# Performance work log

Hardware: AMD Instinct MI355X
Metric: run time of the kernel (lower is better)

## Reference

```python
import jax, jax.numpy as jnp
import numpy as np


def setup_inputs() -> dict:
    key = jax.random.key(0)
    kx, kA, kB, kC, kd = jax.random.split(key, 5)
    d_model, d_state = 2048, 16
    batch, seq_len = 2, 4096
    x = jax.random.normal(kx, (batch, seq_len, d_model), dtype=jnp.float32)
    # HiPPO-style init would be log(arange(1..N)); random positive works for the same math
    A_log = jax.random.uniform(kA, (d_model, d_state), dtype=jnp.float32)
    B = jax.random.normal(kB, (d_model, d_state), dtype=jnp.float32) * 0.02
    C = jax.random.normal(kC, (d_model, d_state), dtype=jnp.float32) * 0.02
    D = jnp.ones((d_model,), dtype=jnp.float32)
    delta = jax.random.uniform(kd, (d_model,), dtype=jnp.float32) * 0.01 + 0.005
    return {"x": x, "A_log": A_log, "B": B, "C": C, "D": D, "delta": delta}


def reference(x, A_log, B, C, D, delta):
    # x: (batch, seq_len, d_model); params per-channel diagonal SSM
    A = -jnp.exp(A_log)                      # (d_model, d_state)
    # zero-order-hold discretization
    A_bar = jnp.exp(delta[:, None] * A)      # (d_model, d_state)
    B_bar = delta[:, None] * B               # (d_model, d_state)

    batch, seq_len, d_model = x.shape
    d_state = A_bar.shape[-1]
    xT = jnp.swapaxes(x, 0, 1)               # (seq_len, batch, d_model)

    def step(h, x_t):
        # h: (batch, d_model, d_state); x_t: (batch, d_model)
        h = A_bar * h + B_bar * x_t[..., None]
        y_t = jnp.einsum('dn,bdn->bd', C, h)
        return h, y_t

    h0 = jnp.zeros((batch, d_model, d_state), dtype=x.dtype)
    _, ys = jax.lax.scan(step, h0, xT)       # ys: (seq_len, batch, d_model)
    y = jnp.swapaxes(ys, 0, 1)
    return y + D * x
```

## Files before the change

### kernel.cpp

```cpp
#include <hip/hip_runtime.h>

#define DM 2048
#define DS 16
#define BATCH 2
#define SEQ 4096
#define P (BATCH * DM)
#define UNR 8


__global__ __launch_bounds__(256) void k_params(const float* __restrict__ A_log,
                                                const float* __restrict__ B,
                                                const float* __restrict__ C,
                                                const float* __restrict__ delta,
                                                float* __restrict__ ws, int Lsteps) {
  int j = blockIdx.x * 256 + threadIdx.x;
  if (j >= DM * DS) return;
  int n = j / DM, d = j - n * DM;
  float dl = delta[d];
  float a = -expf(A_log[d * DS + n]);
  ws[j] = expf(dl * a);
  ws[DS * DM + j] = C[d * DS + n] * dl * B[d * DS + n];
  ws[2 * DS * DM + j] = expf(dl * a * (float)Lsteps);
}

__global__ __launch_bounds__(256) void k_local(const float* __restrict__ x,
                                               const float* __restrict__ ws,
                                               float* __restrict__ Hloc, int Lsteps) {
  int tid = blockIdx.x * 256 + threadIdx.x;
  int p = tid & (P - 1);
  int k = tid >> 12;
  int b = p >> 11;
  int d = p & (DM - 1);
  const float* Abar = ws;
  float ab[DS], g[DS];
#pragma unroll
  for (int n = 0; n < DS; n++) {
    ab[n] = Abar[n * DM + d];
    g[n] = 0.f;
  }
  const float* xp = x + ((size_t)b * SEQ + (size_t)k * Lsteps) * DM + d;
  for (int t = 0; t < Lsteps; t += UNR) {
    float xv[UNR];
#pragma unroll
    for (int j = 0; j < UNR; j++) xv[j] = xp[(size_t)j * DM];
#pragma unroll
    for (int j = 0; j < UNR; j++) {
#pragma unroll
      for (int n = 0; n < DS; n++) g[n] = fmaf(ab[n], g[n], xv[j]);
    }
    xp += (size_t)UNR * DM;
  }
  float* Hp = Hloc + (size_t)(k * DS) * P + p;
#pragma unroll
  for (int n = 0; n < DS; n++) Hp[n * P] = g[n];
}

__global__ __launch_bounds__(256) void k_scan(float* __restrict__ Hloc,
                                              const float* __restrict__ ws, int nc) {
  int tid = blockIdx.x * 256 + threadIdx.x;
  int p = tid & (P - 1);
  int n = tid >> 12;
  int d = p & (DM - 1);
  const float* PowL = ws + 2 * DS * DM;
  float pw = PowL[n * DM + d];
  float carry = 0.f;
  float* Hp = Hloc + (size_t)n * P + p;
  const size_t stride = (size_t)DS * P;
  for (int k0 = 0; k0 < nc; k0 += 16) {
    float v[16];
#pragma unroll
    for (int j = 0; j < 16; j++) v[j] = Hp[(size_t)(k0 + j) * stride];
#pragma unroll
    for (int j = 0; j < 16; j++) {
      Hp[(size_t)(k0 + j) * stride] = carry;
      carry = fmaf(pw, carry, v[j]);
    }
  }
}

__global__ __launch_bounds__(256) void k_final(const float* __restrict__ x,
                                               const float* __restrict__ ws,
                                               const float* __restrict__ Hloc,
                                               const float* __restrict__ Dp,
                                               float* __restrict__ out, int Lsteps) {
  int tid = blockIdx.x * 256 + threadIdx.x;
  int p = tid & (P - 1);
  int k = tid >> 12;
  int b = p >> 11;
  int d = p & (DM - 1);
  const float* Abar = ws;
  const float* CB = ws + DS * DM;
  float ab[DS], cb[DS], g[DS];
#pragma unroll
  for (int n = 0; n < DS; n++) {
    ab[n] = Abar[n * DM + d];
    cb[n] = CB[n * DM + d];
  }
  const float* Hp = Hloc + (size_t)(k * DS) * P + p;
#pragma unroll
  for (int n = 0; n < DS; n++) g[n] = Hp[n * P];
  float Dd = Dp[d];
  size_t off = ((size_t)b * SEQ + (size_t)k * Lsteps) * DM + d;
  const float* xp = x + off;
  float* yp = out + off;
  for (int t = 0; t < Lsteps; t += UNR) {
    float xv[UNR];
#pragma unroll
    for (int j = 0; j < UNR; j++) xv[j] = xp[(size_t)j * DM];
#pragma unroll
    for (int j = 0; j < UNR; j++) {
#pragma unroll
      for (int n = 0; n < DS; n++) g[n] = fmaf(ab[n], g[n], xv[j]);
      float acc = Dd * xv[j];
#pragma unroll
      for (int n = 0; n < DS; n++) acc = fmaf(cb[n], g[n], acc);
      yp[(size_t)j * DM] = acc;
    }
    xp += (size_t)UNR * DM;
    yp += (size_t)UNR * DM;
  }
}

extern "C" void kernel_launch(void* const* d_in, const int* in_sizes, int n_in,
                              void* d_out, int out_size, void* d_ws, size_t ws_size,
                              hipStream_t stream) {
  const float* x = (const float*)d_in[0];
  const float* A_log = (const float*)d_in[1];
  const float* B = (const float*)d_in[2];
  const float* C = (const float*)d_in[3];
  const float* Dp = (const float*)d_in[4];
  const float* delta = (const float*)d_in[5];
  float* out = (float*)d_out;
  float* ws = (float*)d_ws;

  size_t base = 3 * (size_t)DS * DM;
  int nc = 32;
  while (nc > 16 && (base + (size_t)nc * DS * P) * 4 > ws_size) nc >>= 1;
  int Lsteps = SEQ / nc;
  float* Hloc = ws + base;

  k_params<<<(DM * DS + 255) / 256, 256, 0, stream>>>(A_log, B, C, delta, ws, Lsteps);
  k_local<<<(nc * P) / 256, 256, 0, stream>>>(x, ws, Hloc, Lsteps);
  k_scan<<<(DS * P) / 256, 256, 0, stream>>>(Hloc, ws, nc);
  k_final<<<(nc * P) / 256, 256, 0, stream>>>(x, ws, Hloc, Dp, out, Lsteps);
}
```

Baseline: 53.25 us.

## Fuse local, scan and final phases into one cooperative kernel with register-cached x

Merges the three chunked-scan kernels into one cooperative kernel separated by grid-wide syncs. Each thread keeps its 128-step slice of x in registers, so the final pass does not read x from global memory a second time. Two kernel launches go away in exchange for two grid barriers. The 128-float register array per thread raises register pressure and may spill or lower occupancy. If the cooperative launch fails, it falls back to the original three kernels.

```diff
diff --git a/kernel.cpp b/kernel.cpp
--- a/kernel.cpp
+++ b/kernel.cpp
@@ -1,10 +1,14 @@
 #include <hip/hip_runtime.h>
+#include <hip/hip_cooperative_groups.h>
+
+namespace cg = cooperative_groups;
 
 #define DM 2048
 #define DS 16
-#define BATCH 2
 #define SEQ 4096
-#define P (BATCH * DM)
+#define P 4096
+#define NC 32
+#define LST 128
 #define UNR 8
 
 
@@ -12,7 +16,7 @@
                                                 const float* __restrict__ B,
                                                 const float* __restrict__ C,
                                                 const float* __restrict__ delta,
-                                                float* __restrict__ ws, int Lsteps) {
+                                                float* __restrict__ ws) {
   int j = blockIdx.x * 256 + threadIdx.x;
   if (j >= DM * DS) return;
   int n = j / DM, d = j - n * DM;
@@ -20,7 +24,88 @@
   float a = -expf(A_log[d * DS + n]);
   ws[j] = expf(dl * a);
   ws[DS * DM + j] = C[d * DS + n] * dl * B[d * DS + n];
-  ws[2 * DS * DM + j] = expf(dl * a * (float)Lsteps);
+  ws[2 * DS * DM + j] = expf(dl * a * (float)LST);
+}
+
+__global__ __launch_bounds__(256, 2) void k_fused(const float* __restrict__ x,
+                                                  const float* __restrict__ ws,
+                                                  float* __restrict__ Hloc,
+                                                  const float* __restrict__ Dp,
+                                                  float* __restrict__ out) {
+  int bid = blockIdx.x;
+  int k = bid >> 4;
+  int p = ((bid & 15) << 8) + threadIdx.x;
+  int d = p & (DM - 1);
+  int b = p >> 11;
+
+  const float* Abar = ws;
+  float ab[DS];
+#pragma unroll
+  for (int n = 0; n < DS; n++) ab[n] = Abar[n * DM + d];
+
+  const float* xp = x + ((size_t)b * SEQ + (size_t)k * LST) * DM + d;
+  float xr[LST];
+  float g[DS];
+#pragma unroll
+  for (int n = 0; n < DS; n++) g[n] = 0.f;
+#pragma unroll
+  for (int t0 = 0; t0 < LST; t0 += 16) {
+#pragma unroll
+    for (int j = 0; j < 16; j++) xr[t0 + j] = xp[(size_t)(t0 + j) * DM];
+#pragma unroll
+    for (int j = 0; j < 16; j++) {
+#pragma unroll
+      for (int n = 0; n < DS; n++) g[n] = fmaf(ab[n], g[n], xr[t0 + j]);
+    }
+  }
+  float* Hp = Hloc + (size_t)(k * DS) * P + p;
+#pragma unroll
+  for (int n = 0; n < DS; n++) Hp[n * P] = g[n];
+
+  cg::this_grid().sync();
+
+  int tid = bid * 256 + threadIdx.x;
+  if (tid < DS * P) {
+    int pp = tid & (P - 1);
+    int n = tid >> 12;
+    int dd = pp & (DM - 1);
+    const float* PowL = ws + 2 * DS * DM;
+    float pw = PowL[n * DM + dd];
+    float carry = 0.f;
+    float* Sp = Hloc + (size_t)n * P + pp;
+    const size_t stride = (size_t)DS * P;
+#pragma unroll
+    for (int k0 = 0; k0 < NC; k0 += 16) {
+      float v[16];
+#pragma unroll
+      for (int j = 0; j < 16; j++) v[j] = Sp[(size_t)(k0 + j) * stride];
+#pragma unroll
+      for (int j = 0; j < 16; j++) {
+        Sp[(size_t)(k0 + j) * stride] = carry;
+        carry = fmaf(pw, carry, v[j]);
+      }
+    }
+  }
+
+  cg::this_grid().sync();
+
+  const float* CB = ws + DS * DM;
+  float cb[DS];
+#pragma unroll
+  for (int n = 0; n < DS; n++) cb[n] = CB[n * DM + d];
+#pragma unroll
+  for (int n = 0; n < DS; n++) g[n] = Hp[n * P];
+  float Dd = Dp[d];
+  float* yp = out + ((size_t)b * SEQ + (size_t)k * LST) * DM + d;
+#pragma unroll
+  for (int t = 0; t < LST; t++) {
+#pragma unroll
+    for (int n = 0; n < DS; n++) g[n] = fmaf(ab[n], g[n], xr[t]);
+    float acc = Dd * xr[t];
+#pragma unroll
+    for (int n = 0; n < DS; n++) acc = fmaf(cb[n], g[n], acc);
+    yp[(size_t)t * DM] = acc;
+  }
 }
 
 __global__ __launch_bounds__(256) void k_local(const float* __restrict__ x,
@@ -132,15 +217,17 @@
   const float* delta = (const float*)d_in[5];
   float* out = (float*)d_out;
   float* ws = (float*)d_ws;
-
-  size_t base = 3 * (size_t)DS * DM;
-  int nc = 32;
-  while (nc > 16 && (base + (size_t)nc * DS * P) * 4 > ws_size) nc >>= 1;
-  int Lsteps = SEQ / nc;
-  float* Hloc = ws + base;
-
-  k_params<<<(DM * DS + 255) / 256, 256, 0, stream>>>(A_log, B, C, delta, ws, Lsteps);
-  k_local<<<(nc * P) / 256, 256, 0, stream>>>(x, ws, Hloc, Lsteps);
-  k_scan<<<(DS * P) / 256, 256, 0, stream>>>(Hloc, ws, nc);
-  k_final<<<(nc * P) / 256, 256, 0, stream>>>(x, ws, Hloc, Dp, out, Lsteps);
-}
+  float* Hloc = ws + 3 * (size_t)DS * DM;
+
+  k_params<<<(DM * DS + 255) / 256, 256, 0, stream>>>(A_log, B, C, delta, ws);
+
+  void* args[] = {(void*)&x, (void*)&ws, (void*)&Hloc, (void*)&Dp, (void*)&out};
+  hipError_t err = hipLaunchCooperativeKernel((void*)k_fused, dim3(NC * 16), dim3(256),
+                                              args, 0, stream);
+  if (err != hipSuccess) {
+    (void)hipGetLastError();
+    k_local<<<(NC * P) / 256, 256, 0, stream>>>(x, ws, Hloc, LST);
+    k_scan<<<(DS * P) / 256, 256, 0, stream>>>(Hloc, ws, NC);
+    k_final<<<(NC * P) / 256, 256, 0, stream>>>(x, ws, Hloc, Dp, out, LST);
+  }
+}
```

New measurement: 174.4 us. +227.5%, slower.

## Fuse parameter discretization into scan kernels and drop the params launch

Applied to the files above, without the earlier changes.

Removes the separate k_params kernel and recomputes A_bar, C*dl*B and the chunk power inline in each kernel from A_log, B, C and delta, using float4 loads and fast __expf. It also hardcodes the chunk count and length, raises the x-load unroll to 16, and skips writing the last chunk's local state, which the scan never reads. The goal is to save one kernel launch and its dependency on the stream. The cost is redundant exp work per thread and possible small accuracy loss from __expf.

```diff
diff --git a/kernel.cpp b/kernel.cpp
--- a/kernel.cpp
+++ b/kernel.cpp
@@ -2,44 +2,44 @@
 
 #define DM 2048
 #define DS 16
-#define BATCH 2
 #define SEQ 4096
-#define P (BATCH * DM)
-#define UNR 8
+#define P 4096
+#define NC 32
+#define LST 128
+#define UNR 16
 
 
-__global__ __launch_bounds__(256) void k_params(const float* __restrict__ A_log,
-                                                const float* __restrict__ B,
-                                                const float* __restrict__ C,
-                                                const float* __restrict__ delta,
-                                                float* __restrict__ ws, int Lsteps) {
-  int j = blockIdx.x * 256 + threadIdx.x;
-  if (j >= DM * DS) return;
-  int n = j / DM, d = j - n * DM;
-  float dl = delta[d];
-  float a = -expf(A_log[d * DS + n]);
-  ws[j] = expf(dl * a);
-  ws[DS * DM + j] = C[d * DS + n] * dl * B[d * DS + n];
-  ws[2 * DS * DM + j] = expf(dl * a * (float)Lsteps);
+__device__ __forceinline__ void load_ab(const float* __restrict__ A_log, int d,
+                                        float dl, float* ab) {
+  const float4* alp = (const float4*)(A_log + d * DS);
+#pragma unroll
+  for (int q = 0; q < 4; q++) {
+    float4 v = alp[q];
+    ab[4 * q + 0] = __expf(-dl * __expf(v.x));
+    ab[4 * q + 1] = __expf(-dl * __expf(v.y));
+    ab[4 * q + 2] = __expf(-dl * __expf(v.z));
+    ab[4 * q + 3] = __expf(-dl * __expf(v.w));
+  }
 }
 
 __global__ __launch_bounds__(256) void k_local(const float* __restrict__ x,
-                                               const float* __restrict__ ws,
-                                               float* __restrict__ Hloc, int Lsteps) {
+                                               const float* __restrict__ A_log,
+                                               const float* __restrict__ delta,
+                                               float* __restrict__ Hloc) {
   int tid = blockIdx.x * 256 + threadIdx.x;
   int p = tid & (P - 1);
   int k = tid >> 12;
   int b = p >> 11;
   int d = p & (DM - 1);
-  const float* Abar = ws;
+  float dl = delta[d];
   float ab[DS], g[DS];
+  load_ab(A_log, d, dl, ab);
 #pragma unroll
-  for (int n = 0; n < DS; n++) {
-    ab[n] = Abar[n * DM + d];
-    g[n] = 0.f;
-  }
-  const float* xp = x + ((size_t)b * SEQ + (size_t)k * Lsteps) * DM + d;
-  for (int t = 0; t < Lsteps; t += UNR) {
+  for (int n = 0; n < DS; n++) g[n] = 0.f;
+
+  const float* xp = x + ((size_t)b * SEQ + (size_t)k * LST) * DM + d;
+#pragma unroll 1
+  for (int t = 0; t < LST; t += UNR) {
     float xv[UNR];
 #pragma unroll
     for (int j = 0; j < UNR; j++) xv[j] = xp[(size_t)j * DM];
@@ -50,23 +50,27 @@
     }
     xp += (size_t)UNR * DM;
   }
-  float* Hp = Hloc + (size_t)(k * DS) * P + p;
+  if (k < NC - 1) {
+    float* Hp = Hloc + (size_t)(k * DS) * P + p;
 #pragma unroll
-  for (int n = 0; n < DS; n++) Hp[n * P] = g[n];
+    for (int n = 0; n < DS; n++) Hp[n * P] = g[n];
+  }
 }
 
 __global__ __launch_bounds__(256) void k_scan(float* __restrict__ Hloc,
-                                              const float* __restrict__ ws, int nc) {
+                                              const float* __restrict__ A_log,
+                                              const float* __restrict__ delta) {
   int tid = blockIdx.x * 256 + threadIdx.x;
   int p = tid & (P - 1);
   int n = tid >> 12;
   int d = p & (DM - 1);
-  const float* PowL = ws + 2 * DS * DM;
-  float pw = PowL[n * DM + d];
+  float dl = delta[d];
+  float pw = __expf(-dl * __expf(A_log[d * DS + n]) * (float)LST);
   float carry = 0.f;
   float* Hp = Hloc + (size_t)n * P + p;
   const size_t stride = (size_t)DS * P;
-  for (int k0 = 0; k0 < nc; k0 += 16) {
+#pragma unroll
+  for (int k0 = 0; k0 < NC; k0 += 16) {
     float v[16];
 #pragma unroll
     for (int j = 0; j < 16; j++) v[j] = Hp[(size_t)(k0 + j) * stride];
@@ -79,31 +83,43 @@
 }
 
 __global__ __launch_bounds__(256) void k_final(const float* __restrict__ x,
-                                               const float* __restrict__ ws,
+                                               const float* __restrict__ A_log,
+                                               const float* __restrict__ B,
+                                               const float* __restrict__ C,
+                                               const float* __restrict__ Dp,
+                                               const float* __restrict__ delta,
                                                const float* __restrict__ Hloc,
-                                               const float* __restrict__ Dp,
-                                               float* __restrict__ out, int Lsteps) {
+                                               float* __restrict__ out) {
   int tid = blockIdx.x * 256 + threadIdx.x;
   int p = tid & (P - 1);
   int k = tid >> 12;
   int b = p >> 11;
   int d = p & (DM - 1);
-  const float* Abar = ws;
-  const float* CB = ws + DS * DM;
+  float dl = delta[d];
   float ab[DS], cb[DS], g[DS];
+  load_ab(A_log, d, dl, ab);
+  {
+    const float4* bp = (const float4*)(B + d * DS);
+    const float4* cp = (const float4*)(C + d * DS);
 #pragma unroll
-  for (int n = 0; n < DS; n++) {
-    ab[n] = Abar[n * DM + d];
-    cb[n] = CB[n * DM + d];
+    for (int q = 0; q < 4; q++) {
+      float4 bv = bp[q];
+      float4 cv = cp[q];
+      cb[4 * q + 0] = cv.x * dl * bv.x;
+      cb[4 * q + 1] = cv.y * dl * bv.y;
+      cb[4 * q + 2] = cv.z * dl * bv.z;
+      cb[4 * q + 3] = cv.w * dl * bv.w;
+    }
   }
   const float* Hp = Hloc + (size_t)(k * DS) * P + p;
 #pragma unroll
   for (int n = 0; n < DS; n++) g[n] = Hp[n * P];
   float Dd = Dp[d];
-  size_t off = ((size_t)b * SEQ + (size_t)k * Lsteps) * DM + d;
+  size_t off = ((size_t)b * SEQ + (size_t)k * LST) * DM + d;
   const float* xp = x + off;
   float* yp = out + off;
-  for (int t = 0; t < Lsteps; t += UNR) {
+#pragma unroll 1
+  for (int t = 0; t < LST; t += UNR) {
     float xv[UNR];
 #pragma unroll
     for (int j = 0; j < UNR; j++) xv[j] = xp[(size_t)j * DM];
@@ -131,16 +147,9 @@
   const float* Dp = (const float*)d_in[4];
   const float* delta = (const float*)d_in[5];
   float* out = (float*)d_out;
-  float* ws = (float*)d_ws;
+  float* Hloc = (float*)d_ws;
 
-  size_t base = 3 * (size_t)DS * DM;
-  int nc = 32;
-  while (nc > 16 && (base + (size_t)nc * DS * P) * 4 > ws_size) nc >>= 1;
-  int Lsteps = SEQ / nc;
-  float* Hloc = ws + base;
-
-  k_params<<<(DM * DS + 255) / 256, 256, 0, stream>>>(A_log, B, C, delta, ws, Lsteps);
-  k_local<<<(nc * P) / 256, 256, 0, stream>>>(x, ws, Hloc, Lsteps);
-  k_scan<<<(DS * P) / 256, 256, 0, stream>>>(Hloc, ws, nc);
-  k_final<<<(nc * P) / 256, 256, 0, stream>>>(x, ws, Hloc, Dp, out, Lsteps);
+  k_local<<<(NC * P) / 256, 256, 0, stream>>>(x, A_log, delta, Hloc);
+  k_scan<<<(DS * P) / 256, 256, 0, stream>>>(Hloc, A_log, delta);
+  k_final<<<(NC * P) / 256, 256, 0, stream>>>(x, A_log, B, C, Dp, delta, Hloc, out);
 }
```

Measured after the change: 48.02 us. -9.8%, faster.
